# Performance work log

Hardware: AMD Instinct MI355X
Metric: run time of the kernel (lower is better)

Reference implementation:

```python
import jax, jax.numpy as jnp
import numpy as np

A, B, F = 1024, 256, 64  # a: points, b: neighbor/pair dim (contracted), F: feature channels


def setup_inputs() -> dict:
    key = jax.random.key(0)
    k1, k2 = jax.random.split(key)
    tensor = jax.random.normal(k1, (B, F, 3), dtype=jnp.float32)      # l=1 input rep
    f = jax.random.normal(k2, (A, B, F, 3), dtype=jnp.float32)        # l=1 filter rep
    return {"tensor": tensor, "f": f}


def reference(tensor, f):
    # Branch iro==1, fro==1 of EquivariantCombination -> returns [l0_out, l1_out].
    #
    # l0 (_i1f1o0): cg = expand_dims(eye(1), 0) -> shape [1,1,1]; under einsum
    # 'ijk,abfj,bfk->afi' the size-1 i,j,k broadcast, so the result is
    #   out[a,F,0] = sum_b (sum_j f[a,b,F,j]) * (sum_k tensor[b,F,k])
    o0 = jnp.einsum('abf,bf->af', f.sum(-1), tensor.sum(-1))[..., None]  # [A,F,1]
    #
    # l1 (_i1f1o1): eps_ijk f_j t_k is exactly a cross product; sum over b:
    #   out[a,F,i] = sum_b cross(f[a,b,F,:], tensor[b,F,:])_i
    o1 = jnp.cross(f, tensor[None, :, :, :]).sum(axis=1)                  # [A,F,3]
    return (o0, o1)
```

## Files before the change

### kernel.cpp

```cpp
#include <hip/hip_runtime.h>


#define A_DIM 1024
#define B_DIM 256
#define F_DIM 64

__global__ __launch_bounds__(256, 4) void equiv_comb_kernel(
    const float* __restrict__ tensor,
    const float* __restrict__ f,
    float* __restrict__ out)
{
    const int a  = blockIdx.x;
    const int t  = threadIdx.x;
    const int fc = t & 63;
    const int bg = t >> 6;

    const float* __restrict__ fbase = f + (size_t)a * (B_DIM * F_DIM * 3);

    float acc0 = 0.f, c0 = 0.f, c1 = 0.f, c2 = 0.f;

    #pragma unroll 8
    for (int b = bg; b < B_DIM; b += 4) {
        const float* __restrict__ fp = fbase  + (size_t)b * (F_DIM * 3) + fc * 3;
        const float* __restrict__ tp = tensor + (size_t)b * (F_DIM * 3) + fc * 3;
        const float f0 = fp[0], f1 = fp[1], f2 = fp[2];
        const float t0 = tp[0], t1 = tp[1], t2 = tp[2];
        acc0 += (f0 + f1 + f2) * (t0 + t1 + t2);
        c0 += f1 * t2 - f2 * t1;
        c1 += f2 * t0 - f0 * t2;
        c2 += f0 * t1 - f1 * t0;
    }

    __shared__ float red[4][F_DIM][4];
    red[bg][fc][0] = acc0;
    red[bg][fc][1] = c0;
    red[bg][fc][2] = c1;
    red[bg][fc][3] = c2;
    __syncthreads();

    if (t < F_DIM) {
        float s0 = 0.f, s1 = 0.f, s2 = 0.f, s3 = 0.f;
        #pragma unroll
        for (int g = 0; g < 4; ++g) {
            s0 += red[g][t][0];
            s1 += red[g][t][1];
            s2 += red[g][t][2];
            s3 += red[g][t][3];
        }
        out[a * F_DIM + t] = s0;
        float* __restrict__ o1 = out + A_DIM * F_DIM + (size_t)(a * F_DIM + t) * 3;
        o1[0] = s1;
        o1[1] = s2;
        o1[2] = s3;
    }
}

extern "C" void kernel_launch(void* const* d_in, const int* in_sizes, int n_in,
                              void* d_out, int out_size, void* d_ws, size_t ws_size,
                              hipStream_t stream) {
    const float* tensor = (const float*)d_in[0];
    const float* f      = (const float*)d_in[1];
    float* out          = (float*)d_out;

    equiv_comb_kernel<<<dim3(A_DIM), dim3(256), 0, stream>>>(tensor, f, out);
}
```

Before: 285.4 us.

## Vectorize loads to float4 with four features per thread and nontemporal f reads

Each thread now owns four consecutive feature channels and reads them as three 16-byte vector loads from both f and tensor, instead of three scalar strided loads. This is meant to cut instruction count and improve coalescing on the bandwidth-bound stream of f. The f stream is read with nontemporal hints since it is used only once. The block reduction grows to 16 b-slots with a padded shared array, which adds more shared-memory work in the final sum.

```diff
diff --git a/kernel.cpp b/kernel.cpp
--- a/kernel.cpp
+++ b/kernel.cpp
@@ -5,47 +5,77 @@
 #define B_DIM 256
 #define F_DIM 64
 
+typedef float f32x4 __attribute__((ext_vector_type(4)));
+
 __global__ __launch_bounds__(256, 4) void equiv_comb_kernel(
     const float* __restrict__ tensor,
     const float* __restrict__ f,
     float* __restrict__ out)
 {
-    const int a  = blockIdx.x;
-    const int t  = threadIdx.x;
-    const int fc = t & 63;
-    const int bg = t >> 6;
+    const int a     = blockIdx.x;
+    const int t     = threadIdx.x;
+    const int fcg   = t & 15;
+    const int bslot = t >> 4;
 
     const float* __restrict__ fbase = f + (size_t)a * (B_DIM * F_DIM * 3);
 
-    float acc0 = 0.f, c0 = 0.f, c1 = 0.f, c2 = 0.f;
+    float a0[4] = {0.f, 0.f, 0.f, 0.f};
+    float cx[4] = {0.f, 0.f, 0.f, 0.f};
+    float cy[4] = {0.f, 0.f, 0.f, 0.f};
+    float cz[4] = {0.f, 0.f, 0.f, 0.f};
 
-    #pragma unroll 8
-    for (int b = bg; b < B_DIM; b += 4) {
-        const float* __restrict__ fp = fbase  + (size_t)b * (F_DIM * 3) + fc * 3;
-        const float* __restrict__ tp = tensor + (size_t)b * (F_DIM * 3) + fc * 3;
-        const float f0 = fp[0], f1 = fp[1], f2 = fp[2];
-        const float t0 = tp[0], t1 = tp[1], t2 = tp[2];
-        acc0 += (f0 + f1 + f2) * (t0 + t1 + t2);
-        c0 += f1 * t2 - f2 * t1;
-        c1 += f2 * t0 - f0 * t2;
-        c2 += f0 * t1 - f1 * t0;
+    #pragma unroll 2
+    for (int k = 0; k < 16; ++k) {
+        const int b = bslot + (k << 4);
+        const f32x4* __restrict__ fp =
+            reinterpret_cast<const f32x4*>(fbase  + (size_t)b * (F_DIM * 3) + fcg * 12);
+        const f32x4* __restrict__ tp =
+            reinterpret_cast<const f32x4*>(tensor + (size_t)b * (F_DIM * 3) + fcg * 12);
+
+        const f32x4 fl0 = __builtin_nontemporal_load(fp + 0);
+        const f32x4 fl1 = __builtin_nontemporal_load(fp + 1);
+        const f32x4 fl2 = __builtin_nontemporal_load(fp + 2);
+        const f32x4 tl0 = tp[0];
+        const f32x4 tl1 = tp[1];
+        const f32x4 tl2 = tp[2];
+
+        const float fv[12] = {fl0.x, fl0.y, fl0.z, fl0.w,
+                              fl1.x, fl1.y, fl1.z, fl1.w,
+                              fl2.x, fl2.y, fl2.z, fl2.w};
+        const float tv[12] = {tl0.x, tl0.y, tl0.z, tl0.w,
+                              tl1.x, tl1.y, tl1.z, tl1.w,
+                              tl2.x, tl2.y, tl2.z, tl2.w};
+
+        #pragma unroll
+        for (int q = 0; q < 4; ++q) {
+            const float f0 = fv[q * 3 + 0], f1 = fv[q * 3 + 1], f2 = fv[q * 3 + 2];
+            const float t0 = tv[q * 3 + 0], t1 = tv[q * 3 + 1], t2 = tv[q * 3 + 2];
+            a0[q] += (f0 + f1 + f2) * (t0 + t1 + t2);
+            cx[q] += f1 * t2 - f2 * t1;
+            cy[q] += f2 * t0 - f0 * t2;
+            cz[q] += f0 * t1 - f1 * t0;
+        }
     }
 
-    __shared__ float red[4][F_DIM][4];
-    red[bg][fc][0] = acc0;
-    red[bg][fc][1] = c0;
-    red[bg][fc][2] = c1;
-    red[bg][fc][3] = c2;
+    __shared__ float red[16][F_DIM][5];
+    #pragma unroll
+    for (int q = 0; q < 4; ++q) {
+        const int fc = fcg * 4 + q;
+        red[bslot][fc][0] = a0[q];
+        red[bslot][fc][1] = cx[q];
+        red[bslot][fc][2] = cy[q];
+        red[bslot][fc][3] = cz[q];
+    }
     __syncthreads();
 
     if (t < F_DIM) {
         float s0 = 0.f, s1 = 0.f, s2 = 0.f, s3 = 0.f;
         #pragma unroll
-        for (int g = 0; g < 4; ++g) {
-            s0 += red[g][t][0];
-            s1 += red[g][t][1];
-            s2 += red[g][t][2];
-            s3 += red[g][t][3];
+        for (int s = 0; s < 16; ++s) {
+            s0 += red[s][t][0];
+            s1 += red[s][t][1];
+            s2 += red[s][t][2];
+            s3 += red[s][t][3];
         }
         out[a * F_DIM + t] = s0;
         float* __restrict__ o1 = out + A_DIM * F_DIM + (size_t)(a * F_DIM + t) * 3;
```

Result: faster. 279.2 us (-2.2%).
